# Kernel optimization log

Measured on AMD Instinct MI355X. Metric: run time of the kernel, lower is better.

## Reference

```python
import jax, jax.numpy as jnp
import numpy as np

HEADS = 16

def rotate_half(x):
    x1, x2 = jnp.split(x, 2, axis=-1)
    return jnp.concatenate((-x2, x1), axis=-1)

def setup_inputs() -> dict:
    key = jax.random.key(0)
    k1, k2, k3, k4 = jax.random.split(key, 4)
    b, n, h = 2, 2048, 1024
    d = h // HEADS
    x = jax.random.normal(k1, (b, n, h), dtype=jnp.float32)
    rotary_emb = jax.random.normal(k2, (n, d), dtype=jnp.float32)
    w_qkv = jax.random.normal(k3, (h, 3 * h), dtype=jnp.float32) * (1.0 / np.sqrt(h))
    w_out = jax.random.normal(k4, (h, h), dtype=jnp.float32) * (1.0 / np.sqrt(h))
    return {"x": x, "rotary_emb": rotary_emb, "w_qkv": w_qkv, "w_out": w_out}

def reference(x, rotary_emb, w_qkv, w_out):
    b, n, hidden = x.shape
    d = hidden // HEADS
    # fused QKV projection: [b,n,3*hidden]
    qkv = jnp.einsum('bnh,hk->bnk', x, w_qkv)
    q, k, v = jnp.split(qkv, 3, axis=-1)
    # [b,n,hidden] -> [b,H,n,d]
    split_heads = lambda t: t.reshape(b, n, HEADS, d).transpose(0, 2, 1, 3)
    q, k, v = split_heads(q), split_heads(k), split_heads(v)
    # rotary: pos is [n,d], broadcast over batch/heads
    cos = jnp.cos(rotary_emb)[None, None]
    sin = jnp.sin(rotary_emb)[None, None]
    q = q * cos + rotate_half(q) * sin
    k = k * cos + rotate_half(k) * sin
    # SDPA (no mask, no dropout)
    scale = 1.0 / np.sqrt(d).astype(np.float32)
    scores = jnp.einsum('bhqd,bhkd->bhqk', q, k) * scale
    attn = jax.nn.softmax(scores, axis=-1)
    out = jnp.einsum('bhqk,bhkd->bhqd', attn, v)
    out = out.transpose(0, 2, 1, 3).reshape(b, n, hidden)
    return jnp.einsum('bnh,hk->bnk', out, w_out)
```

## Files before the change

### kernel.cpp

```cpp
#include <hip/hip_runtime.h>
#include <math.h>

#define HEADS 16
#define DH    64
#define SEQ   2048
#define HID   1024
#define NROW  4096

typedef __attribute__((ext_vector_type(8))) short bf16x8;
typedef __attribute__((ext_vector_type(4))) short bf16x4;
typedef __attribute__((ext_vector_type(4))) float f32x4;

#define AS1 __attribute__((address_space(1)))
#define AS3 __attribute__((address_space(3)))

#define QSCALE 0.18033688011112042f

__device__ __forceinline__ unsigned short f2bf(float x) {
    unsigned int u = __builtin_bit_cast(unsigned int, x);
    u = (u + 0x7FFFu + ((u >> 16) & 1u)) >> 16;
    return (unsigned short)u;
}

__device__ __forceinline__ void gload_lds16(const unsigned short* g, unsigned short* l) {
    __builtin_amdgcn_global_load_lds((AS1 void*)g, (AS3 void*)l, 16, 0, 0);
}

__device__ void wtrans_body(const float* __restrict__ wsrc, unsigned short* __restrict__ wt,
                            int K, int N, int bx, int by, float (*T)[65])
{
    const int tid = threadIdx.x;
    const int k0 = by * 64, n0 = bx * 64;
    #pragma unroll
    for (int rnd = 0; rnd < 4; ++rnd) {
        int row = (tid >> 4) + rnd * 16;
        int c = (tid & 15) * 4;
        float4 v = *(const float4*)&wsrc[(size_t)(k0 + row) * N + n0 + c];
        T[row][c] = v.x; T[row][c+1] = v.y; T[row][c+2] = v.z; T[row][c+3] = v.w;
    }
    __syncthreads();
    const int sr = tid >> 3, sc = (tid & 7) << 3;
    #pragma unroll
    for (int half = 0; half < 2; ++half) {
        int n = sr + half * 32;
        union { unsigned short u[8]; bf16x8 v; } pk;
        #pragma unroll
        for (int j = 0; j < 8; ++j) pk.u[j] = f2bf(T[sc + j][n]);
        *(bf16x8*)&wt[(size_t)(n0 + n) * K + k0 + sc] = pk.v;
    }
}

__global__ __launch_bounds__(256) void prep(const float* __restrict__ x,
                                            const float* __restrict__ rot,
                                            const float* __restrict__ w_qkv,
                                            const float* __restrict__ w_out,
                                            unsigned short* __restrict__ xb,
                                            float2* __restrict__ ctab,
                                            unsigned short* __restrict__ wqkvT,
                                            unsigned short* __restrict__ woutT)
{
    __shared__ float T[64][65];
    const int bid = blockIdx.x;
    if (bid < 2048) {
        size_t i = ((size_t)bid * 256 + threadIdx.x) * 8;
        float4 a = *(const float4*)&x[i];
        float4 b = *(const float4*)&x[i + 4];
        union { unsigned short u[8]; bf16x8 v; } pk;
        pk.u[0] = f2bf(a.x); pk.u[1] = f2bf(a.y); pk.u[2] = f2bf(a.z); pk.u[3] = f2bf(a.w);
        pk.u[4] = f2bf(b.x); pk.u[5] = f2bf(b.y); pk.u[6] = f2bf(b.z); pk.u[7] = f2bf(b.w);
        *(bf16x8*)&xb[i] = pk.v;
    } else if (bid < 2560) {
        int i = (bid - 2048) * 256 + threadIdx.x;
        float r = rot[i];
        float s, c;
        __sincosf(r, &s, &c);
        ctab[i] = make_float2(c, s);
    } else if (bid < 3328) {
        int idx = bid - 2560;
        wtrans_body(w_qkv, wqkvT, 1024, 3072, idx % 48, idx / 48, T);
    } else {
        int idx = bid - 3328;
        wtrans_body(w_out, woutT, 1024, 1024, idx % 16, idx / 16, T);
    }
}

__global__ __launch_bounds__(256) void gemm_qkv(const unsigned short* __restrict__ A,
                                                const unsigned short* __restrict__ Bt,
                                                const float2* __restrict__ ctab,
                                                unsigned short* __restrict__ qb,
                                                unsigned short* __restrict__ kb,
                                                unsigned short* __restrict__ vt)
{
    __shared__ __align__(16) unsigned short As[2][128 * 32];
    __shared__ __align__(16) unsigned short Bs[2][128 * 32];
    const int tid = threadIdx.x;
    const int w = tid >> 6, lane = tid & 63;
    const int quad = lane >> 4, lm = lane & 15;
    const int wr = (w >> 1) * 64, wc = (w & 1) * 64;
    const int bm = blockIdx.y * 128, bn = blockIdx.x * 128;
    const int m0 = tid >> 2;
    const int sk = (((tid & 3) ^ ((m0 >> 1) & 3)) << 3);
    const int kx = ((quad ^ ((lm >> 1) & 3)) << 3);

    f32x4 acc[4][4];
    #pragma unroll
    for (int i = 0; i < 4; ++i)
        #pragma unroll
        for (int j = 0; j < 4; ++j) acc[i][j] = (f32x4){0.f, 0.f, 0.f, 0.f};

    gload_lds16(&A [(size_t)(bm + m0     ) * 1024 + sk], &As[0][w * 512]);
    gload_lds16(&A [(size_t)(bm + m0 + 64) * 1024 + sk], &As[0][2048 + w * 512]);
    gload_lds16(&Bt[(size_t)(bn + m0     ) * 1024 + sk], &Bs[0][w * 512]);
    gload_lds16(&Bt[(size_t)(bn + m0 + 64) * 1024 + sk], &Bs[0][2048 + w * 512]);

    #pragma unroll 2
    for (int it = 0; it < 32; ++it) {
        const int buf = it & 1;
        __syncthreads();
        {
            const int nk = ((it + 1) & 31) * 32;
            gload_lds16(&A [(size_t)(bm + m0     ) * 1024 + nk + sk], &As[buf ^ 1][w * 512]);
            gload_lds16(&A [(size_t)(bm + m0 + 64) * 1024 + nk + sk], &As[buf ^ 1][2048 + w * 512]);
            gload_lds16(&Bt[(size_t)(bn + m0     ) * 1024 + nk + sk], &Bs[buf ^ 1][w * 512]);
            gload_lds16(&Bt[(size_t)(bn + m0 + 64) * 1024 + nk + sk], &Bs[buf ^ 1][2048 + w * 512]);
        }
        bf16x8 af[4], bfr[4];
        #pragma unroll
        for (int mt = 0; mt < 4; ++mt) af[mt] = *(const bf16x8*)&As[buf][(wr + mt * 16 + lm) * 32 + kx];
        #pragma unroll
        for (int nt = 0; nt < 4; ++nt) bfr[nt] = *(const bf16x8*)&Bs[buf][(wc + nt * 16 + lm) * 32 + kx];
        #pragma unroll
        for (int mt = 0; mt < 4; ++mt)
            #pragma unroll
            for (int nt = 0; nt < 4; ++nt)
                acc[mt][nt] = __builtin_amdgcn_mfma_f32_16x16x32_bf16(af[mt], bfr[nt], acc[mt][nt], 0, 0, 0);
    }

    const int colbase = bn + wc;
    const int region = colbase >> 10;
    const int h = (colbase >> 6) & 15;

    if (region == 2) {
        #pragma unroll
        for (int mt = 0; mt < 4; ++mt) {
            int rowb = bm + wr + mt * 16 + quad * 4;
            int b = rowb >> 11, seq = rowb & (SEQ - 1);
            int t = seq >> 5, ks = seq & 31;
            #pragma unroll
            for (int nt = 0; nt < 4; ++nt) {
                int d = nt * 16 + lm;
                int ksw = (((ks >> 2) ^ (lm & 7)) << 2);
                ushort4 pk;
                pk.x = f2bf(acc[mt][nt][0]); pk.y = f2bf(acc[mt][nt][1]);
                pk.z = f2bf(acc[mt][nt][2]); pk.w = f2bf(acc[mt][nt][3]);
                *(ushort4*)&vt[(((size_t)(b * HEADS + h) * 64 + t) * 64 + d) * 32 + ksw] = pk;
            }
        }
    } else {
        const float qs = (region == 0) ? QSCALE : 1.0f;
        unsigned short* dst = (region == 0) ? qb : kb;
        #pragma unroll
        for (int mt = 0; mt < 4; ++mt) {
            #pragma unroll
            for (int nt = 0; nt < 2; ++nt) {
                int d = nt * 16 + lm;
                #pragma unroll
                for (int r = 0; r < 4; ++r) {
                    int row = bm + wr + mt * 16 + quad * 4 + r;
                    int b = row >> 11, seq = row & (SEQ - 1);
                    float2 cs0 = ctab[seq * DH + d];
                    float2 cs1 = ctab[seq * DH + d + 32];
                    float x0 = acc[mt][nt][r];
                    float x1 = acc[mt][nt + 2][r];
                    size_t ob = ((size_t)(b * HEADS + h) * SEQ + seq) * DH;
                    dst[ob + d]      = f2bf((x0 * cs0.x - x1 * cs0.y) * qs);
                    dst[ob + d + 32] = f2bf((x1 * cs1.x + x0 * cs1.y) * qs);
                }
            }
        }
    }
}

__global__ __launch_bounds__(256, 4) void attn13(const unsigned short* __restrict__ qb,
                                                 const unsigned short* __restrict__ kb,
                                                 const unsigned short* __restrict__ vt,
                                                 unsigned short* __restrict__ attnb)
{
    __shared__ __align__(16) char smem[32768];
    unsigned short* Ks = (unsigned short*)smem;
    unsigned short* Vs = (unsigned short*)(smem + 16384);

    const int tid = threadIdx.x;
    const int w = tid >> 6, lane = tid & 63, quad = lane >> 4, lm = lane & 15;
    const int qg = w >> 1, kg = w & 1;

    const int L = blockIdx.x + blockIdx.y * 32;
    const int bh = (L & 7) + 8 * ((L >> 3) & 3);
    const int q0 = (L >> 5) * 64;

    const int b = bh >> 4, h = bh & 15;
    const size_t hb = (size_t)bh * SEQ * DH;

    bf16x8 qf[2][2];
    #pragma unroll
    for (int qt = 0; qt < 2; ++qt)
        #pragma unroll
        for (int c = 0; c < 2; ++c)
            qf[qt][c] = *(const bf16x8*)&qb[hb + (size_t)(q0 + qg * 32 + qt * 16 + lm) * DH + c * 32 + quad * 8];

    const int r0 = (w * 16) + (lane >> 3);
    const int p0 = lane & 7;
    const int gk0 = r0 * 64 + (p0 ^ (r0 & 7)) * 8;
    const int r1 = r0 + 8;
    const int gk1 = r1 * 64 + (p0 ^ (r1 & 7)) * 8;
    const unsigned short* kgp = kb + hb;
    const unsigned short* vgp = vt + hb;
    const int gv0 = w * 1024 + lane * 8;
    const int gv1 = gv0 + 512;
    unsigned short* kdst0 = Ks + w * 1024;
    unsigned short* kdst1 = Ks + w * 1024 + 512;
    unsigned short* vdst0 = Vs + w * 1024;
    unsigned short* vdst1 = Vs + w * 1024 + 512;

    int kfo[2];
    #pragma unroll
    for (int c = 0; c < 2; ++c)
        kfo[c] = (kg * 32 + lm) * 64 + (((c * 4 + quad) ^ (lm & 7)) * 8);
    const int vrow = kg * 2048 + lm * 32;

    float rs[2] = {0.f, 0.f};
    f32x4 o[2][4];
    #pragma unroll
    for (int qt = 0; qt < 2; ++qt)
        #pragma unroll
        for (int dt = 0; dt < 4; ++dt) o[qt][dt] = (f32x4){0.f, 0.f, 0.f, 0.f};

    gload_lds16(kgp + gk0, kdst0);
    gload_lds16(kgp + gk1, kdst1);
    gload_lds16(vgp + gv0, vdst0);
    gload_lds16(vgp + gv1, vdst1);

    #pragma unroll 2
    for (int it = 0; it < 32; ++it) {
        const int buf = it & 1;
        __syncthreads();
        {
            const size_t nb = (size_t)((it + 1) & 31) * 4096;
            const int bo = (buf ^ 1) * 4096;
            gload_lds16(kgp + nb + gk0, kdst0 + bo);
            gload_lds16(kgp + nb + gk1, kdst1 + bo);
            gload_lds16(vgp + nb + gv0, vdst0 + bo);
            gload_lds16(vgp + nb + gv1, vdst1 + bo);
        }
        const unsigned short* Kb = Ks + buf * 4096;
        const unsigned short* Vb = Vs + buf * 4096;

        #pragma unroll
        for (int kt = 0; kt < 2; ++kt) {
            bf16x8 k0 = *(const bf16x8*)&Kb[kfo[0] + kt * 1024];
            bf16x8 k1 = *(const bf16x8*)&Kb[kfo[1] + kt * 1024];
            bf16x4 vb[4];
            #pragma unroll
            for (int dt = 0; dt < 4; ++dt)
                vb[dt] = *(const bf16x4*)&Vb[vrow + dt * 512 + (((kt * 4 + quad) ^ (lm & 7)) << 2)];
            f32x4 s[2];
            #pragma unroll
            for (int qt = 0; qt < 2; ++qt) {
                f32x4 z = (f32x4){0.f, 0.f, 0.f, 0.f};
                z = __builtin_amdgcn_mfma_f32_16x16x32_bf16(k0, qf[qt][0], z, 0, 0, 0);
                s[qt] = __builtin_amdgcn_mfma_f32_16x16x32_bf16(k1, qf[qt][1], z, 0, 0, 0);
            }
            #pragma unroll
            for (int qt = 0; qt < 2; ++qt) {
                unsigned int u[4];
                #pragma unroll
                for (int r = 0; r < 4; ++r) {
                    float p = __builtin_amdgcn_exp2f(s[qt][r]);
                    rs[qt] += p;
                    u[r] = __builtin_bit_cast(unsigned int, p);
                }
                union { unsigned int w2[2]; bf16x4 v; } pk;
                pk.w2[0] = __builtin_amdgcn_perm(u[1], u[0], 0x07060302);
                pk.w2[1] = __builtin_amdgcn_perm(u[3], u[2], 0x07060302);
                #pragma unroll
                for (int dt = 0; dt < 4; ++dt)
                    o[qt][dt] = __builtin_amdgcn_mfma_f32_16x16x16bf16_1k(pk.v, vb[dt], o[qt][dt], 0, 0, 0);
            }
        }
    }

    #pragma unroll
    for (int off = 16; off < 64; off <<= 1)
        #pragma unroll
        for (int qt = 0; qt < 2; ++qt) rs[qt] += __shfl_xor(rs[qt], off, 64);

    __syncthreads();
    float* oBuf = (float*)smem;
    float* lRed = (float*)(smem + 17408);
    if (kg == 1) {
        #pragma unroll
        for (int qt = 0; qt < 2; ++qt)
            #pragma unroll
            for (int dt = 0; dt < 4; ++dt)
                #pragma unroll
                for (int r = 0; r < 4; ++r)
                    oBuf[(qg * 32 + qt * 16 + quad * 4 + r) * 68 + dt * 16 + lm] = o[qt][dt][r];
        if (quad == 0) {
            #pragma unroll
            for (int qt = 0; qt < 2; ++qt) lRed[qg * 32 + qt * 16 + lm] = rs[qt];
        }
    }
    __syncthreads();
    if (kg == 0) {
        #pragma unroll
        for (int qt = 0; qt < 2; ++qt) {
            rs[qt] += lRed[qg * 32 + qt * 16 + lm];
            #pragma unroll
            for (int dt = 0; dt < 4; ++dt)
                #pragma unroll
                for (int r = 0; r < 4; ++r)
                    o[qt][dt][r] += oBuf[(qg * 32 + qt * 16 + quad * 4 + r) * 68 + dt * 16 + lm];
        }
        #pragma unroll
        for (int qt = 0; qt < 2; ++qt)
            #pragma unroll
            for (int r = 0; r < 4; ++r) {
                float inv = 1.0f / __shfl(rs[qt], quad * 4 + r, 64);
                int row = b * SEQ + q0 + qg * 32 + qt * 16 + quad * 4 + r;
                #pragma unroll
                for (int dt = 0; dt < 4; ++dt)
                    attnb[(size_t)row * HID + h * DH + dt * 16 + lm] = f2bf(o[qt][dt][r] * inv);
            }
    }
}

__global__ __launch_bounds__(256) void gemm_out(const unsigned short* __restrict__ A,
                                                const unsigned short* __restrict__ Bt,
                                                float* __restrict__ C)
{
    __shared__ __align__(16) unsigned short As[2][64 * 32];
    __shared__ __align__(16) unsigned short Bs[2][128 * 32];
    const int tid = threadIdx.x;
    const int w = tid >> 6, lane = tid & 63;
    const int quad = lane >> 4, lm = lane & 15;
    const int wr = (w >> 1) * 32, wc = (w & 1) * 64;
    const int bm = blockIdx.y * 64, bn = blockIdx.x * 128;
    const int m0 = tid >> 2;
    const int sk = (((tid & 3) ^ ((m0 >> 1) & 3)) << 3);
    const int kx = ((quad ^ ((lm >> 1) & 3)) << 3);

    f32x4 acc[2][4];
    #pragma unroll
    for (int i = 0; i < 2; ++i)
        #pragma unroll
        for (int j = 0; j < 4; ++j) acc[i][j] = (f32x4){0.f, 0.f, 0.f, 0.f};

    gload_lds16(&A [(size_t)(bm + m0     ) * 1024 + sk], &As[0][w * 512]);
    gload_lds16(&Bt[(size_t)(bn + m0     ) * 1024 + sk], &Bs[0][w * 512]);
    gload_lds16(&Bt[(size_t)(bn + m0 + 64) * 1024 + sk], &Bs[0][2048 + w * 512]);

    #pragma unroll 2
    for (int it = 0; it < 32; ++it) {
        const int buf = it & 1;
        __syncthreads();
        {
            const int nk = ((it + 1) & 31) * 32;
            gload_lds16(&A [(size_t)(bm + m0     ) * 1024 + nk + sk], &As[buf ^ 1][w * 512]);
            gload_lds16(&Bt[(size_t)(bn + m0     ) * 1024 + nk + sk], &Bs[buf ^ 1][w * 512]);
            gload_lds16(&Bt[(size_t)(bn + m0 + 64) * 1024 + nk + sk], &Bs[buf ^ 1][2048 + w * 512]);
        }
        bf16x8 af[2], bfr[4];
        #pragma unroll
        for (int mt = 0; mt < 2; ++mt) af[mt] = *(const bf16x8*)&As[buf][(wr + mt * 16 + lm) * 32 + kx];
        #pragma unroll
        for (int nt = 0; nt < 4; ++nt) bfr[nt] = *(const bf16x8*)&Bs[buf][(wc + nt * 16 + lm) * 32 + kx];
        #pragma unroll
        for (int mt = 0; mt < 2; ++mt)
            #pragma unroll
            for (int nt = 0; nt < 4; ++nt)
                acc[mt][nt] = __builtin_amdgcn_mfma_f32_16x16x32_bf16(af[mt], bfr[nt], acc[mt][nt], 0, 0, 0);
    }

    #pragma unroll
    for (int mt = 0; mt < 2; ++mt)
        #pragma unroll
        for (int nt = 0; nt < 4; ++nt) {
            int col = bn + wc + nt * 16 + lm;
            #pragma unroll
            for (int r = 0; r < 4; ++r) {
                int row = bm + wr + mt * 16 + quad * 4 + r;
                C[(size_t)row * 1024 + col] = acc[mt][nt][r];
            }
        }
}

extern "C" void kernel_launch(void* const* d_in, const int* in_sizes, int n_in,
                              void* d_out, int out_size, void* d_ws, size_t ws_size,
                              hipStream_t stream) {
    const float* x     = (const float*)d_in[0];
    const float* rot   = (const float*)d_in[1];
    const float* w_qkv = (const float*)d_in[2];
    const float* w_out = (const float*)d_in[3];
    float* out = (float*)d_out;

    char* ws = (char*)d_ws;
    unsigned short* xb    = (unsigned short*)(ws);
    unsigned short* qb    = (unsigned short*)(ws + (size_t)( 8u << 20));
    unsigned short* kb    = (unsigned short*)(ws + (size_t)(16u << 20));
    unsigned short* vt    = (unsigned short*)(ws + (size_t)(24u << 20));
    unsigned short* attnb = (unsigned short*)(ws + (size_t)(32u << 20));
    unsigned short* wqkvT = (unsigned short*)(ws + (size_t)(40u << 20));
    unsigned short* woutT = (unsigned short*)(ws + (size_t)(46u << 20));
    float2*         ctab  = (float2*)        (ws + (size_t)(48u << 20));

    prep<<<3584, 256, 0, stream>>>(x, rot, w_qkv, w_out, xb, ctab, wqkvT, woutT);

    gemm_qkv<<<dim3(24, 32), 256, 0, stream>>>(xb, wqkvT, ctab, qb, kb, vt);

    attn13<<<dim3(32, 32), 256, 0, stream>>>(qb, kb, vt, attnb);

    gemm_out<<<dim3(8, 64), 256, 0, stream>>>(attnb, woutT, out);
}
```

Baseline: 202.0 us.

## Shrink QKV GEMM tile to 128x64, drop double buffering, raise occupancy

The QKV projection GEMM moves from 128x128 tiles with double-buffered LDS to 128x64 tiles with one LDS buffer and two barriers per k-step. Each wave now owns a 32x64 slice, and launch bounds request 6 blocks per CU. The grid doubles to 1536 blocks to fill more CUs and hide latency through occupancy rather than software prefetch. The cost is that loads no longer overlap compute within a block, and operand reuse per tile is lower.

```diff
diff --git a/kernel.cpp b/kernel.cpp
--- a/kernel.cpp
+++ b/kernel.cpp
@@ -84,65 +84,55 @@
     }
 }
 
-__global__ __launch_bounds__(256) void gemm_qkv(const unsigned short* __restrict__ A,
-                                                const unsigned short* __restrict__ Bt,
-                                                const float2* __restrict__ ctab,
-                                                unsigned short* __restrict__ qb,
-                                                unsigned short* __restrict__ kb,
-                                                unsigned short* __restrict__ vt)
+__global__ __launch_bounds__(256, 6) void gemm_qkv(const unsigned short* __restrict__ A,
+                                                   const unsigned short* __restrict__ Bt,
+                                                   const float2* __restrict__ ctab,
+                                                   unsigned short* __restrict__ qb,
+                                                   unsigned short* __restrict__ kb,
+                                                   unsigned short* __restrict__ vt)
 {
-    __shared__ __align__(16) unsigned short As[2][128 * 32];
-    __shared__ __align__(16) unsigned short Bs[2][128 * 32];
+    __shared__ __align__(16) unsigned short As[128 * 32];
+    __shared__ __align__(16) unsigned short Bs[64 * 32];
     const int tid = threadIdx.x;
     const int w = tid >> 6, lane = tid & 63;
     const int quad = lane >> 4, lm = lane & 15;
-    const int wr = (w >> 1) * 64, wc = (w & 1) * 64;
-    const int bm = blockIdx.y * 128, bn = blockIdx.x * 128;
+    const int wr = w * 32;
+    const int bm = blockIdx.y * 128, bn = blockIdx.x * 64;
     const int m0 = tid >> 2;
     const int sk = (((tid & 3) ^ ((m0 >> 1) & 3)) << 3);
     const int kx = ((quad ^ ((lm >> 1) & 3)) << 3);
 
-    f32x4 acc[4][4];
-    #pragma unroll
-    for (int i = 0; i < 4; ++i)
+    f32x4 acc[2][4];
+    #pragma unroll
+    for (int i = 0; i < 2; ++i)
         #pragma unroll
         for (int j = 0; j < 4; ++j) acc[i][j] = (f32x4){0.f, 0.f, 0.f, 0.f};
 
-    gload_lds16(&A [(size_t)(bm + m0     ) * 1024 + sk], &As[0][w * 512]);
-    gload_lds16(&A [(size_t)(bm + m0 + 64) * 1024 + sk], &As[0][2048 + w * 512]);
-    gload_lds16(&Bt[(size_t)(bn + m0     ) * 1024 + sk], &Bs[0][w * 512]);
-    gload_lds16(&Bt[(size_t)(bn + m0 + 64) * 1024 + sk], &Bs[0][2048 + w * 512]);
-
-    #pragma unroll 2
-    for (int it = 0; it < 32; ++it) {
-        const int buf = it & 1;
+    for (int k0 = 0; k0 < 1024; k0 += 32) {
         __syncthreads();
-        {
-            const int nk = ((it + 1) & 31) * 32;
-            gload_lds16(&A [(size_t)(bm + m0     ) * 1024 + nk + sk], &As[buf ^ 1][w * 512]);
-            gload_lds16(&A [(size_t)(bm + m0 + 64) * 1024 + nk + sk], &As[buf ^ 1][2048 + w * 512]);
-            gload_lds16(&Bt[(size_t)(bn + m0     ) * 1024 + nk + sk], &Bs[buf ^ 1][w * 512]);
-            gload_lds16(&Bt[(size_t)(bn + m0 + 64) * 1024 + nk + sk], &Bs[buf ^ 1][2048 + w * 512]);
-        }
-        bf16x8 af[4], bfr[4];
-        #pragma unroll
-        for (int mt = 0; mt < 4; ++mt) af[mt] = *(const bf16x8*)&As[buf][(wr + mt * 16 + lm) * 32 + kx];
-        #pragma unroll
-        for (int nt = 0; nt < 4; ++nt) bfr[nt] = *(const bf16x8*)&Bs[buf][(wc + nt * 16 + lm) * 32 + kx];
-        #pragma unroll
-        for (int mt = 0; mt < 4; ++mt)
+        gload_lds16(&A [(size_t)(bm + m0     ) * 1024 + k0 + sk], As + w * 512);
+        gload_lds16(&A [(size_t)(bm + m0 + 64) * 1024 + k0 + sk], As + 2048 + w * 512);
+        gload_lds16(&Bt[(size_t)(bn + m0     ) * 1024 + k0 + sk], Bs + w * 512);
+        __syncthreads();
+        bf16x8 af[2], bfr[4];
+        #pragma unroll
+        for (int mt = 0; mt < 2; ++mt) af[mt] = *(const bf16x8*)&As[(wr + mt * 16 + lm) * 32 + kx];
+        #pragma unroll
+        for (int nt = 0; nt < 4; ++nt) bfr[nt] = *(const bf16x8*)&Bs[(nt * 16 + lm) * 32 + kx];
+        #pragma unroll
+        for (int mt = 0; mt < 2; ++mt)
             #pragma unroll
             for (int nt = 0; nt < 4; ++nt)
                 acc[mt][nt] = __builtin_amdgcn_mfma_f32_16x16x32_bf16(af[mt], bfr[nt], acc[mt][nt], 0, 0, 0);
     }
 
-    const int colbase = bn + wc;
+    const int colbase = bn;
     const int region = colbase >> 10;
     const int h = (colbase >> 6) & 15;
 
     if (region == 2) {
         #pragma unroll
-        for (int mt = 0; mt < 4; ++mt) {
+        for (int mt = 0; mt < 2; ++mt) {
             int rowb = bm + wr + mt * 16 + quad * 4;
             int b = rowb >> 11, seq = rowb & (SEQ - 1);
             int t = seq >> 5, ks = seq & 31;
@@ -160,7 +150,7 @@
         const float qs = (region == 0) ? QSCALE : 1.0f;
         unsigned short* dst = (region == 0) ? qb : kb;
         #pragma unroll
-        for (int mt = 0; mt < 4; ++mt) {
+        for (int mt = 0; mt < 2; ++mt) {
             #pragma unroll
             for (int nt = 0; nt < 2; ++nt) {
                 int d = nt * 16 + lm;
@@ -415,7 +405,7 @@
 
     prep<<<3584, 256, 0, stream>>>(x, rot, w_qkv, w_out, xb, ctab, wqkvT, woutT);
 
-    gemm_qkv<<<dim3(24, 32), 256, 0, stream>>>(xb, wqkvT, ctab, qb, kb, vt);
+    gemm_qkv<<<dim3(48, 32), 256, 0, stream>>>(xb, wqkvT, ctab, qb, kb, vt);
 
     attn13<<<dim3(32, 32), 256, 0, stream>>>(qb, kb, vt, attnb);
 
```

Result: faster. 193.7 us (-4.1%).
